# Kernel optimization log

Measured on AMD Instinct MI355X. Metric: run time of the kernel, lower is better.

The kernel has to match this reference:

```python
import jax, jax.numpy as jnp
import numpy as np

NUM_SEGMENTS = 1024  # number of distinct group ids in ix (fill_max)
DIM = 384


def setup_inputs() -> dict:
    key = jax.random.key(0)
    ks = jax.random.split(key, 8)
    H = 65536
    x = jax.random.normal(ks[0], (1, H, DIM), dtype=jnp.float32)
    ix = jax.random.randint(ks[1], (1, H), 0, NUM_SEGMENTS, dtype=jnp.int64)
    s = 0.05  # keep g(x) in a numerically tame range before exp
    f_w = jax.random.normal(ks[2], (DIM, DIM), dtype=jnp.float32) * s
    f_b = jax.random.normal(ks[3], (DIM,), dtype=jnp.float32) * s
    g_w = jax.random.normal(ks[4], (DIM, DIM), dtype=jnp.float32) * s
    g_b = jax.random.normal(ks[5], (DIM,), dtype=jnp.float32) * s
    h_w = jax.random.normal(ks[6], (DIM, DIM), dtype=jnp.float32) * s
    h_b = jax.random.normal(ks[7], (DIM,), dtype=jnp.float32) * s
    return {"x": x, "ix": ix, "f_w": f_w, "f_b": f_b, "g_w": g_w,
            "g_b": g_b, "h_w": h_w, "h_b": h_b}


def reference(x, ix, f_w, f_b, g_w, g_b, h_w, h_b):
    # x: [1, H, C]; ix: [1, H] group ids. Original builds an [H,H] equality
    # mask; the math is exactly a per-group softmax(g(x))-weighted sum of f(x)
    # broadcast back to every member of the group, so we use segment_sum.
    ix0 = ix[0]                                   # [H]
    fx = x[0] @ f_w.T + f_b                       # [H, C]
    gx = jnp.clip(x[0] @ g_w.T + g_b, -50.0, 50.0)
    w = jnp.exp(gx)                               # [H, C]
    denom = jax.ops.segment_sum(w, ix0, num_segments=NUM_SEGMENTS)  # [S, C]
    denom = jnp.maximum(denom, 1e-9)
    wi = w / denom[ix0]                           # normalized weights, [H, C]
    num = jax.ops.segment_sum(fx * wi, ix0, num_segments=NUM_SEGMENTS)  # [S, C]
    y = num[ix0][None]                            # [1, H, C]
    return y @ h_w.T + h_b
```

## Files before the change

kernel.cpp:

```cpp
#include <hip/hip_runtime.h>

#define DIM 384
#define NSEG 1024
#define CHUNK 64
#define LDA 392
#define MAXLS 16

typedef __attribute__((ext_vector_type(8))) short bf16x8;
typedef __attribute__((ext_vector_type(4))) float f32x4;

static __device__ __forceinline__ short f2bf(float f) {
    union { float f; unsigned u; } v{f};
    unsigned r = (v.u + 0x7FFFu + ((v.u >> 16) & 1u)) >> 16;
    return (short)r;
}

#define PACK_BLOCKS ((2 * 24 * 12 * 64) / 256)

__global__ void prep_kernel(const int* __restrict__ ix, int* __restrict__ hist,
                            const float* __restrict__ fw, const float* __restrict__ gw,
                            short* __restrict__ pb, int H) {
    int b = blockIdx.x;
    if (b < PACK_BLOCKS) {
        int idx = b * 256 + threadIdx.x;
        int lane = idx & 63;
        int ks   = (idx >> 6) % 12;
        int T    = ((idx >> 6) / 12) % 24;
        int mat  = idx / (64 * 12 * 24);
        const float* src = mat ? gw : fw;
        int ch = T * 16 + (lane & 15);
        int k0 = ks * 32 + (lane >> 4) * 8;
        short* dst = pb + (size_t)idx * 8;
#pragma unroll
        for (int e = 0; e < 8; e++) dst[e] = f2bf(src[(size_t)ch * DIM + k0 + e]);
    } else {
        int i = (b - PACK_BLOCKS) * 256 + threadIdx.x;
        if (i < H) atomicAdd(&hist[ix[i]], 1);
    }
}


__global__ void scan_kernel(const int* __restrict__ hist, int* __restrict__ seg_start,
                            int* __restrict__ cursor) {
    __shared__ int tmp[NSEG];
    int t = threadIdx.x;
    int v = hist[t];
    tmp[t] = v;
    __syncthreads();
    for (int off = 1; off < NSEG; off <<= 1) {
        int add = (t >= off) ? tmp[t - off] : 0;
        __syncthreads();
        tmp[t] += add;
        __syncthreads();
    }
    int incl = tmp[t];
    seg_start[t] = incl - v;
    cursor[t]    = incl - v;
    if (t == NSEG - 1) seg_start[NSEG] = incl;
}

__global__ void scatter_kernel(const int* __restrict__ ix, int* __restrict__ cursor,
                               int* __restrict__ order, int H) {
    int i = blockIdx.x * blockDim.x + threadIdx.x;
    if (i < H) {
        int p = atomicAdd(&cursor[ix[i]], 1);
        order[p] = i;
    }
}

__global__ __launch_bounds__(1024) void seg_gemm_chunk(
    const float* __restrict__ x, const short* __restrict__ pb,
    const float* __restrict__ f_b, const float* __restrict__ g_b,
    const int* __restrict__ order, const int* __restrict__ ix,
    float* __restrict__ den_acc, float* __restrict__ num_acc) {
    const int chunk0 = blockIdx.x * CHUNK;
    const int tid  = threadIdx.x;
    const int lane = tid & 63;
    const int wave = tid >> 6;
    const int n    = lane & 15;
    const int q    = lane >> 4;
    const int pair = wave & 7;
    const int half = wave >> 3;
    const int cb   = pair * 48;

    __shared__ short As[CHUNK * LDA];
    __shared__ int   segrow[CHUNK];

    {
        int r  = tid >> 4;
        int c6 = tid & 15;
        int gr = order[chunk0 + r];
        if (c6 == 0) segrow[r] = ix[gr];
        const f32x4* xr = (const f32x4*)(x + (size_t)gr * DIM);
        short* dst = &As[r * LDA];
#pragma unroll
        for (int i = 0; i < 6; i++) {
            f32x4 v = __builtin_nontemporal_load(xr + c6 + 16 * i);
            short4 s = { f2bf(v[0]), f2bf(v[1]), f2bf(v[2]), f2bf(v[3]) };
            *(short4*)&dst[(c6 + 16 * i) * 4] = s;
        }
    }
    __syncthreads();

    float fbv[3], gbv[3];
#pragma unroll
    for (int t = 0; t < 3; t++) {
        fbv[t] = f_b[cb + t * 16 + n];
        gbv[t] = g_b[cb + t * 16 + n];
    }

    f32x4 accf[2][3], accg[2][3];
#pragma unroll
    for (int rt = 0; rt < 2; rt++)
#pragma unroll
        for (int t = 0; t < 3; t++) {
            accf[rt][t] = (f32x4){0.f, 0.f, 0.f, 0.f};
            accg[rt][t] = (f32x4){0.f, 0.f, 0.f, 0.f};
        }

#pragma unroll
    for (int ks = 0; ks < 12; ks++) {
        bf16x8 a[2];
#pragma unroll
        for (int rt = 0; rt < 2; rt++)
            a[rt] = *(const bf16x8*)&As[((half * 2 + rt) * 16 + n) * LDA + ks * 32 + q * 8];
#pragma unroll
        for (int t = 0; t < 3; t++) {
            int Tg = pair * 3 + t;
            bf16x8 bfr = *(const bf16x8*)(pb + ((size_t)((0 * 24 + Tg) * 12 + ks)) * 512 + lane * 8);
            bf16x8 bgr = *(const bf16x8*)(pb + ((size_t)((1 * 24 + Tg) * 12 + ks)) * 512 + lane * 8);
#pragma unroll
            for (int rt = 0; rt < 2; rt++) {
                accf[rt][t] = __builtin_amdgcn_mfma_f32_16x16x32_bf16(a[rt], bfr, accf[rt][t], 0, 0, 0);
                accg[rt][t] = __builtin_amdgcn_mfma_f32_16x16x32_bf16(a[rt], bgr, accg[rt][t], 0, 0, 0);
            }
        }
    }

    const int s0 = segrow[0];
    __syncthreads();
    float* accs = (float*)As;
    for (int i = tid; i < MAXLS * DIM * 2; i += 1024) accs[i] = 0.f;
    __syncthreads();

#pragma unroll
    for (int t = 0; t < 3; t++) {
        int ch = cb + t * 16 + n;
        float rw = 0.f, rf = 0.f;
        int cur = -1;
#pragma unroll
        for (int rt = 0; rt < 2; rt++) {
#pragma unroll
            for (int r = 0; r < 4; r++) {
                int m  = (half * 2 + rt) * 16 + q * 4 + r;
                int ls = segrow[m] - s0;
                if (ls != cur) {
                    if (cur >= 0) {
                        if (cur < MAXLS) {
                            atomicAdd(&accs[(cur * DIM + ch) * 2 + 0], rw);
                            atomicAdd(&accs[(cur * DIM + ch) * 2 + 1], rf);
                        } else {
                            atomicAdd(&den_acc[(size_t)(s0 + cur) * DIM + ch], rw);
                            atomicAdd(&num_acc[(size_t)(s0 + cur) * DIM + ch], rf);
                        }
                    }
                    cur = ls; rw = 0.f; rf = 0.f;
                }
                float gx = accg[rt][t][r] + gbv[t];
                gx = fmaxf(-50.f, fminf(50.f, gx));
                float w = __expf(gx);
                rw += w;
                rf += (accf[rt][t][r] + fbv[t]) * w;
            }
        }
        if (cur < MAXLS) {
            atomicAdd(&accs[(cur * DIM + ch) * 2 + 0], rw);
            atomicAdd(&accs[(cur * DIM + ch) * 2 + 1], rf);
        } else {
            atomicAdd(&den_acc[(size_t)(s0 + cur) * DIM + ch], rw);
            atomicAdd(&num_acc[(size_t)(s0 + cur) * DIM + ch], rf);
        }
    }
    __syncthreads();

    int nls = segrow[CHUNK - 1] - s0 + 1;
    if (nls > MAXLS) nls = MAXLS;
    for (int i = tid; i < nls * DIM; i += 1024) {
        int ls = i / DIM, ch = i - ls * DIM;
        float dw = accs[(ls * DIM + ch) * 2 + 0];
        float dn = accs[(ls * DIM + ch) * 2 + 1];
        if (dw != 0.f || dn != 0.f) {
            atomicAdd(&den_acc[(size_t)(s0 + ls) * DIM + ch], dw);
            atomicAdd(&num_acc[(size_t)(s0 + ls) * DIM + ch], dn);
        }
    }
}

__global__ __launch_bounds__(256) void hgemm_kernel(
    const float* __restrict__ num, const float* __restrict__ den,
    const float* __restrict__ h_w, const float* __restrict__ h_b,
    float* __restrict__ z) {
    const int m0 = blockIdx.x * 64;
    const int c0 = blockIdx.y * 64;
    const int tid = threadIdx.x;
    const int ty = tid >> 4, tx = tid & 15;
    __shared__ float As[16][64];
    __shared__ float Bs[16][64];
    float acc[4][4];
#pragma unroll
    for (int i = 0; i < 4; i++)
#pragma unroll
        for (int j = 0; j < 4; j++) acc[i][j] = 0.f;

    for (int k0 = 0; k0 < DIM; k0 += 16) {
        __syncthreads();
        {
            int m  = tid >> 2;
            int kq = (tid & 3) << 2;
            size_t idx = (size_t)(m0 + m) * DIM + k0 + kq;
            float4 v = *(const float4*)(num + idx);
            float4 d = *(const float4*)(den + idx);
            v.x /= fmaxf(d.x, 1e-9f); v.y /= fmaxf(d.y, 1e-9f);
            v.z /= fmaxf(d.z, 1e-9f); v.w /= fmaxf(d.w, 1e-9f);
            As[kq + 0][m] = v.x; As[kq + 1][m] = v.y;
            As[kq + 2][m] = v.z; As[kq + 3][m] = v.w;
            float4 w = *(const float4*)(h_w + (size_t)(c0 + m) * DIM + k0 + kq);
            Bs[kq + 0][m] = w.x; Bs[kq + 1][m] = w.y;
            Bs[kq + 2][m] = w.z; Bs[kq + 3][m] = w.w;
        }
        __syncthreads();
#pragma unroll
        for (int kk = 0; kk < 16; kk++) {
            float4 a4 = *(const float4*)&As[kk][ty * 4];
            float4 b4 = *(const float4*)&Bs[kk][tx * 4];
            float a[4] = { a4.x, a4.y, a4.z, a4.w };
            float b[4] = { b4.x, b4.y, b4.z, b4.w };
#pragma unroll
            for (int i = 0; i < 4; i++)
#pragma unroll
                for (int j = 0; j < 4; j++) acc[i][j] += a[i] * b[j];
        }
    }
#pragma unroll
    for (int i = 0; i < 4; i++)
#pragma unroll
        for (int j = 0; j < 4; j++)
            z[(size_t)(m0 + ty * 4 + i) * DIM + c0 + tx * 4 + j] = acc[i][j] + h_b[c0 + tx * 4 + j];
}

__global__ void gather_kernel(const int* __restrict__ ix, const f32x4* __restrict__ z,
                              f32x4* __restrict__ out, int H) {
    int t = blockIdx.x * blockDim.x + threadIdx.x;
    int total = H * (DIM / 4);
    if (t < total) {
        int i = t / (DIM / 4);
        int qq = t - i * (DIM / 4);
        f32x4 v = z[(size_t)ix[i] * (DIM / 4) + qq];
        __builtin_nontemporal_store(v, out + (size_t)i * (DIM / 4) + qq);
    }
}

extern "C" void kernel_launch(void* const* d_in, const int* in_sizes, int n_in,
                              void* d_out, int out_size, void* d_ws, size_t ws_size,
                              hipStream_t stream) {
    const float* x   = (const float*)d_in[0];
    const int*   ix  = (const int*)d_in[1];
    const float* f_w = (const float*)d_in[2];
    const float* f_b = (const float*)d_in[3];
    const float* g_w = (const float*)d_in[4];
    const float* g_b = (const float*)d_in[5];
    const float* h_w = (const float*)d_in[6];
    const float* h_b = (const float*)d_in[7];
    float* out = (float*)d_out;
    const int H = in_sizes[0] / DIM;

    char* w = (char*)d_ws;
    int* hist      = (int*)w;   w += 4096;
    int* seg_start = (int*)w;   w += 8192;
    int* cursor    = (int*)w;   w += 4096;
    int* order     = (int*)w;   w += (size_t)H * 4;
    float* den_acc = (float*)w; w += (size_t)NSEG * DIM * 4;
    float* num_acc = (float*)w; w += (size_t)NSEG * DIM * 4;
    float* z       = (float*)w; w += (size_t)NSEG * DIM * 4;
    short* pb      = (short*)w;

    (void)hipMemsetAsync(hist, 0, NSEG * sizeof(int), stream);
    (void)hipMemsetAsync(den_acc, 0, (size_t)2 * NSEG * DIM * 4, stream);
    prep_kernel<<<PACK_BLOCKS + (H + 255) / 256, 256, 0, stream>>>(ix, hist, f_w, g_w, pb, H);
    scan_kernel<<<1, NSEG, 0, stream>>>(hist, seg_start, cursor);
    scatter_kernel<<<(H + 255) / 256, 256, 0, stream>>>(ix, cursor, order, H);
    seg_gemm_chunk<<<H / CHUNK, 1024, 0, stream>>>(x, pb, f_b, g_b, order, ix,
                                                   den_acc, num_acc);
    hgemm_kernel<<<dim3(NSEG / 64, DIM / 64), 256, 0, stream>>>(num_acc, den_acc,
                                                                h_w, h_b, z);
    gather_kernel<<<(H * (DIM / 4) + 255) / 256, 256, 0, stream>>>(
        ix, (const f32x4*)z, (f32x4*)out, H);
}
```

Measured before the change: 338.5 us.

## Privatize histogram/scatter in LDS, shuffle scan, halve GEMM chunk to 32 rows

The histogram now uses per-block LDS histograms written to partial buffers, which removes the memset and the global atomics. The scan is rebuilt with wave shuffles, and the scatter takes block-level bases through one atomic per segment per block before scattering with LDS counters. The segment GEMM uses 32-row chunks with 512 threads and 4 blocks per CU, so each wave covers all rows for its channel slice and more blocks run concurrently. The trade-off is that each pb weight fragment is reloaded across twice as many blocks, and the scatter now runs on only 16 blocks.

```diff
diff --git a/kernel.cpp b/kernel.cpp
--- a/kernel.cpp
+++ b/kernel.cpp
@@ -2,9 +2,10 @@
 
 #define DIM 384
 #define NSEG 1024
-#define CHUNK 64
+#define CHUNK 32
 #define LDA 392
-#define MAXLS 16
+#define MAXLS 8
+#define NHB 16
 
 typedef __attribute__((ext_vector_type(8))) short bf16x8;
 typedef __attribute__((ext_vector_type(4))) float f32x4;
@@ -15,14 +16,17 @@
     return (short)r;
 }
 
-#define PACK_BLOCKS ((2 * 24 * 12 * 64) / 256)
-
-__global__ void prep_kernel(const int* __restrict__ ix, int* __restrict__ hist,
-                            const float* __restrict__ fw, const float* __restrict__ gw,
-                            short* __restrict__ pb, int H) {
+#define PACKB ((2 * 24 * 12 * 64) / 1024)
+
+__global__ __launch_bounds__(1024) void prep_kernel(
+    const int* __restrict__ ix, int* __restrict__ hist_part,
+    const float* __restrict__ fw, const float* __restrict__ gw,
+    short* __restrict__ pb, int H) {
+    __shared__ int lh[NSEG];
     int b = blockIdx.x;
-    if (b < PACK_BLOCKS) {
-        int idx = b * 256 + threadIdx.x;
+    int t = threadIdx.x;
+    if (b < PACKB) {
+        int idx = b * 1024 + t;
         int lane = idx & 63;
         int ks   = (idx >> 6) % 12;
         int T    = ((idx >> 6) / 12) % 24;
@@ -34,41 +38,80 @@
 #pragma unroll
         for (int e = 0; e < 8; e++) dst[e] = f2bf(src[(size_t)ch * DIM + k0 + e]);
     } else {
-        int i = (b - PACK_BLOCKS) * 256 + threadIdx.x;
-        if (i < H) atomicAdd(&hist[ix[i]], 1);
-    }
-}
-
-
-__global__ void scan_kernel(const int* __restrict__ hist, int* __restrict__ seg_start,
-                            int* __restrict__ cursor) {
-    __shared__ int tmp[NSEG];
+        int hb = b - PACKB;
+        lh[t] = 0;
+        __syncthreads();
+        int rpb = (H + NHB - 1) / NHB;
+        int lo = hb * rpb;
+        int hi = lo + rpb; if (hi > H) hi = H;
+        for (int i = lo + t; i < hi; i += 1024)
+            atomicAdd(&lh[ix[i]], 1);
+        __syncthreads();
+        hist_part[hb * NSEG + t] = lh[t];
+    }
+}
+
+__global__ __launch_bounds__(1024) void scan_kernel(
+    const int* __restrict__ hist_part, int* __restrict__ seg_start,
+    int* __restrict__ cursor) {
+    __shared__ int wsum[16];
     int t = threadIdx.x;
-    int v = hist[t];
-    tmp[t] = v;
-    __syncthreads();
-    for (int off = 1; off < NSEG; off <<= 1) {
-        int add = (t >= off) ? tmp[t - off] : 0;
-        __syncthreads();
-        tmp[t] += add;
-        __syncthreads();
-    }
-    int incl = tmp[t];
+    int v = 0;
+#pragma unroll
+    for (int b = 0; b < NHB; b++) v += hist_part[b * NSEG + t];
+    int lane = t & 63, wv = t >> 6;
+    int s = v;
+#pragma unroll
+    for (int off = 1; off < 64; off <<= 1) {
+        int u = __shfl_up(s, off, 64);
+        if (lane >= off) s += u;
+    }
+    if (lane == 63) wsum[wv] = s;
+    __syncthreads();
+    if (wv == 0) {
+        int ws = (lane < 16) ? wsum[lane] : 0;
+#pragma unroll
+        for (int off = 1; off < 16; off <<= 1) {
+            int u = __shfl_up(ws, off, 64);
+            if (lane >= off) ws += u;
+        }
+        if (lane < 16) wsum[lane] = ws;
+    }
+    __syncthreads();
+    int incl = s + (wv ? wsum[wv - 1] : 0);
     seg_start[t] = incl - v;
     cursor[t]    = incl - v;
     if (t == NSEG - 1) seg_start[NSEG] = incl;
 }
 
-__global__ void scatter_kernel(const int* __restrict__ ix, int* __restrict__ cursor,
-                               int* __restrict__ order, int H) {
-    int i = blockIdx.x * blockDim.x + threadIdx.x;
-    if (i < H) {
-        int p = atomicAdd(&cursor[ix[i]], 1);
+__global__ __launch_bounds__(1024) void scatter_kernel(
+    const int* __restrict__ ix, int* __restrict__ cursor,
+    int* __restrict__ order, int H) {
+    __shared__ int lbase[NSEG];
+    __shared__ int lcur[NSEG];
+    int t = threadIdx.x;
+    int rpb = (H + gridDim.x - 1) / gridDim.x;
+    int lo = blockIdx.x * rpb;
+    int hi = lo + rpb; if (hi > H) hi = H;
+    lbase[t] = 0;
+    __syncthreads();
+    for (int i = lo + t; i < hi; i += 1024)
+        atomicAdd(&lbase[ix[i]], 1);
+    __syncthreads();
+    int c = lbase[t];
+    int base = (c > 0) ? atomicAdd(&cursor[t], c) : 0;
+    __syncthreads();
+    lbase[t] = base;
+    lcur[t] = 0;
+    __syncthreads();
+    for (int i = lo + t; i < hi; i += 1024) {
+        int sg = ix[i];
+        int p = lbase[sg] + atomicAdd(&lcur[sg], 1);
         order[p] = i;
     }
 }
 
-__global__ __launch_bounds__(1024) void seg_gemm_chunk(
+__global__ __launch_bounds__(512, 4) void seg_gemm_chunk(
     const float* __restrict__ x, const short* __restrict__ pb,
     const float* __restrict__ f_b, const float* __restrict__ g_b,
     const int* __restrict__ order, const int* __restrict__ ix,
@@ -79,9 +122,7 @@
     const int wave = tid >> 6;
     const int n    = lane & 15;
     const int q    = lane >> 4;
-    const int pair = wave & 7;
-    const int half = wave >> 3;
-    const int cb   = pair * 48;
+    const int cb   = wave * 48;
 
     __shared__ short As[CHUNK * LDA];
     __shared__ int   segrow[CHUNK];
@@ -123,10 +164,10 @@
         bf16x8 a[2];
 #pragma unroll
         for (int rt = 0; rt < 2; rt++)
-            a[rt] = *(const bf16x8*)&As[((half * 2 + rt) * 16 + n) * LDA + ks * 32 + q * 8];
+            a[rt] = *(const bf16x8*)&As[(rt * 16 + n) * LDA + ks * 32 + q * 8];
 #pragma unroll
         for (int t = 0; t < 3; t++) {
-            int Tg = pair * 3 + t;
+            int Tg = wave * 3 + t;
             bf16x8 bfr = *(const bf16x8*)(pb + ((size_t)((0 * 24 + Tg) * 12 + ks)) * 512 + lane * 8);
             bf16x8 bgr = *(const bf16x8*)(pb + ((size_t)((1 * 24 + Tg) * 12 + ks)) * 512 + lane * 8);
 #pragma unroll
@@ -140,7 +181,7 @@
     const int s0 = segrow[0];
     __syncthreads();
     float* accs = (float*)As;
-    for (int i = tid; i < MAXLS * DIM * 2; i += 1024) accs[i] = 0.f;
+    for (int i = tid; i < MAXLS * DIM * 2; i += 512) accs[i] = 0.f;
     __syncthreads();
 
 #pragma unroll
@@ -152,7 +193,7 @@
         for (int rt = 0; rt < 2; rt++) {
 #pragma unroll
             for (int r = 0; r < 4; r++) {
-                int m  = (half * 2 + rt) * 16 + q * 4 + r;
+                int m  = rt * 16 + q * 4 + r;
                 int ls = segrow[m] - s0;
                 if (ls != cur) {
                     if (cur >= 0) {
@@ -185,7 +226,7 @@
 
     int nls = segrow[CHUNK - 1] - s0 + 1;
     if (nls > MAXLS) nls = MAXLS;
-    for (int i = tid; i < nls * DIM; i += 1024) {
+    for (int i = tid; i < nls * DIM; i += 512) {
         int ls = i / DIM, ch = i - ls * DIM;
         float dw = accs[(ls * DIM + ch) * 2 + 0];
         float dn = accs[(ls * DIM + ch) * 2 + 1];
@@ -275,7 +316,7 @@
     const int H = in_sizes[0] / DIM;
 
     char* w = (char*)d_ws;
-    int* hist      = (int*)w;   w += 4096;
+    int* hist_part = (int*)w;   w += NHB * NSEG * 4;
     int* seg_start = (int*)w;   w += 8192;
     int* cursor    = (int*)w;   w += 4096;
     int* order     = (int*)w;   w += (size_t)H * 4;
@@ -284,13 +325,12 @@
     float* z       = (float*)w; w += (size_t)NSEG * DIM * 4;
     short* pb      = (short*)w;
 
-    (void)hipMemsetAsync(hist, 0, NSEG * sizeof(int), stream);
     (void)hipMemsetAsync(den_acc, 0, (size_t)2 * NSEG * DIM * 4, stream);
-    prep_kernel<<<PACK_BLOCKS + (H + 255) / 256, 256, 0, stream>>>(ix, hist, f_w, g_w, pb, H);
-    scan_kernel<<<1, NSEG, 0, stream>>>(hist, seg_start, cursor);
-    scatter_kernel<<<(H + 255) / 256, 256, 0, stream>>>(ix, cursor, order, H);
-    seg_gemm_chunk<<<H / CHUNK, 1024, 0, stream>>>(x, pb, f_b, g_b, order, ix,
-                                                   den_acc, num_acc);
+    prep_kernel<<<PACKB + NHB, 1024, 0, stream>>>(ix, hist_part, f_w, g_w, pb, H);
+    scan_kernel<<<1, NSEG, 0, stream>>>(hist_part, seg_start, cursor);
+    scatter_kernel<<<NHB, 1024, 0, stream>>>(ix, cursor, order, H);
+    seg_gemm_chunk<<<H / CHUNK, 512, 0, stream>>>(x, pb, f_b, g_b, order, ix,
+                                                  den_acc, num_acc);
     hgemm_kernel<<<dim3(NSEG / 64, DIM / 64), 256, 0, stream>>>(num_acc, den_acc,
                                                                 h_w, h_b, z);
     gather_kernel<<<(H * (DIM / 4) + 255) / 256, 256, 0, stream>>>(
```

New measurement: 312.6 us. -7.7%, faster.
